# Kernel optimization log

Hardware: AMD Instinct MI355X
Metric: run time of the kernel (lower is better)

The kernel has to match this reference:

```python
import jax, jax.numpy as jnp
import numpy as np

HEAD_DIM = 256
ROTARY_DIM = 128  # max(2, int(0.5*256) rounded down to even)
HALF_ROT = ROTARY_DIM // 2   # 64
HALF_HEAD = HEAD_DIM // 2    # 128
WAVELENGTH = 10000.0
ROPE_SCALING = 1.0
SOFT_CAP = 50.0
EPS = 1e-6
NQ = 8
NKV = 4
GROUPS = NQ // NKV
NEG_INF = -1e9


def rms_norm(x, scale):
    # keras-hub Gemma RMSNorm: fp32 compute, out = x * rsqrt(mean(x^2)+eps) * (1+scale)
    x32 = x.astype(jnp.float32)
    var = jnp.mean(jnp.square(x32), axis=-1, keepdims=True)
    y = x32 * jax.lax.rsqrt(var + EPS)
    return (y * (1.0 + scale.astype(jnp.float32))).astype(x.dtype)


def l2_norm(x):
    # Gemma4VNorm: pure L2 normalization over head_dim, no learned scale
    x32 = x.astype(jnp.float32)
    ss = jnp.sum(jnp.square(x32), axis=-1, keepdims=True)
    return (x32 * jax.lax.rsqrt(ss + EPS)).astype(x.dtype)


def apply_partial_rope(x):
    # x: [B, S, N, HEAD_DIM]. Partial proportional rotation: only the first
    # HALF_ROT elements of each HALF_HEAD half get rotated. RoPE inverse freqs
    # use denominator_dim = HEAD_DIM (not rotary_dim).
    S = x.shape[1]
    inv_freq = 1.0 / (WAVELENGTH ** (jnp.arange(0, ROTARY_DIM, 2, dtype=jnp.float32) / HEAD_DIM))  # [HALF_ROT]
    pos = jnp.arange(S, dtype=jnp.float32) / ROPE_SCALING
    freq = pos[:, None] * inv_freq[None, :]             # [S, HALF_ROT]
    cos = jnp.cos(freq)[None, :, None, :].astype(x.dtype)
    sin = jnp.sin(freq)[None, :, None, :].astype(x.dtype)
    x1 = x[..., :HALF_HEAD]
    x2 = x[..., HALF_HEAD:]
    x1r, x1n = x1[..., :HALF_ROT], x1[..., HALF_ROT:]
    x2r, x2n = x2[..., :HALF_ROT], x2[..., HALF_ROT:]
    # rotate-half form: [x1r, x2r]*cos + [-x2r, x1r]*sin
    y1r = x1r * cos - x2r * sin
    y2r = x2r * cos + x1r * sin
    return jnp.concatenate([y1r, x1n, y2r, x2n], axis=-1)


def setup_inputs() -> dict:
    key = jax.random.key(0)
    ks = jax.random.split(key, 6)
    B, S, D = 2, 2048, 2048
    x = jax.random.normal(ks[0], (B, S, D), jnp.float32)
    # causal mask [B, S, S]
    attention_mask = jnp.broadcast_to(jnp.tril(jnp.ones((S, S), bool))[None], (B, S, S))
    w_scale = 0.02
    Wq = jax.random.normal(ks[1], (NQ, D, HEAD_DIM), jnp.float32) * w_scale
    Wk = jax.random.normal(ks[2], (NKV, D, HEAD_DIM), jnp.float32) * w_scale
    Wv = jax.random.normal(ks[3], (NKV, D, HEAD_DIM), jnp.float32) * w_scale
    Wo = jax.random.normal(ks[4], (NQ, HEAD_DIM, D), jnp.float32) * w_scale
    q_scale = jnp.zeros((HEAD_DIM,), jnp.float32)
    k_scale = jnp.zeros((HEAD_DIM,), jnp.float32)
    return {"x": x, "attention_mask": attention_mask, "Wq": Wq, "Wk": Wk,
            "Wv": Wv, "Wo": Wo, "q_scale": q_scale, "k_scale": k_scale}


def reference(x, attention_mask, Wq, Wk, Wv, Wo, q_scale, k_scale):
    B, S, D = x.shape
    q = jnp.einsum('btd,ndh->btnh', x, Wq)
    q = apply_partial_rope(rms_norm(q, q_scale))
    k = jnp.einsum('bsd,kdh->bskh', x, Wk)
    k = apply_partial_rope(rms_norm(k, k_scale))
    v = l2_norm(jnp.einsum('bsd,kdh->bskh', x, Wv))
    # grouped-query attention, scaling = 1.0 (Gemma4 relies on QK norm)
    qg = q.reshape(B, S, NKV, GROUPS, HEAD_DIM)
    logits = jnp.einsum('btkgh,bskh->bkgts', qg, k)
    # logit soft cap
    logits = jnp.tanh(logits / SOFT_CAP) * SOFT_CAP
    mask = attention_mask[:, None, None, :, :]
    logits = jnp.where(mask, logits, NEG_INF)
    probs = jax.nn.softmax(logits.astype(jnp.float32), axis=-1).astype(logits.dtype)
    out = jnp.einsum('bkgts,bskh->btkgh', probs, v).reshape(B, S, NQ, HEAD_DIM)
    return jnp.einsum('btnh,nhd->btd', out, Wo)
```

## Files before the change

kernel.cpp:

```cpp
#include <hip/hip_runtime.h>

#define AS1 __attribute__((address_space(1)))
#define AS3 __attribute__((address_space(3)))

typedef __attribute__((ext_vector_type(8))) _Float16 f16x8;
typedef __attribute__((ext_vector_type(4))) _Float16 f16x4;
typedef __attribute__((ext_vector_type(4))) float f32x4;

#define MFMA_K16(a, b, c) __builtin_amdgcn_mfma_f32_16x16x16f16(a, b, c, 0, 0, 0)

__device__ __forceinline__ unsigned short f2h(float f) {
    union { _Float16 h; unsigned short u; } v; v.h = (_Float16)f; return v.u;
}

__device__ __forceinline__ void gload16(const void* g, void* l) {
    __builtin_amdgcn_global_load_lds((const AS1 unsigned int*)g, (AS3 unsigned int*)l, 16, 0, 0);
}

#define GBAR() __builtin_amdgcn_s_barrier()
#define VM4()  asm volatile("s_waitcnt vmcnt(4)" ::: "memory")
#define VM0()  asm volatile("s_waitcnt vmcnt(0)" ::: "memory")

__global__ __launch_bounds__(256) void k_prep(const float* __restrict__ x,
                                              const float* __restrict__ Wq,
                                              const float* __restrict__ Wk,
                                              const float* __restrict__ Wv,
                                              const float* __restrict__ Wo,
                                              unsigned short* __restrict__ xh,
                                              unsigned short* __restrict__ WT,
                                              unsigned short* __restrict__ WoT) {
    int z = blockIdx.z;
    if (z == 24) {
        int blk = blockIdx.y * 8 + blockIdx.x;
        int t = threadIdx.y * 32 + threadIdx.x;
        const float4* s4 = (const float4*)x;
        ushort4* d4 = (ushort4*)xh;
        int base = blk * 4096 + t;
#pragma unroll
        for (int i = 0; i < 16; i++) {
            float4 v = s4[base + i * 256];
            ushort4 u;
            u.x = f2h(v.x); u.y = f2h(v.y); u.z = f2h(v.z); u.w = f2h(v.w);
            d4[base + i * 256] = u;
        }
        return;
    }
    const float* src; unsigned short* dst;
    int ld_src, c0, r0;
    if (z < 16) {
        if (z < 8)       { src = Wq + (size_t)z * 524288;        dst = WT + (size_t)z * 524288; }
        else if (z < 12) { src = Wk + (size_t)(z - 8) * 524288;  dst = WT + (size_t)2048 * 2048 + (size_t)(z - 8) * 524288; }
        else             { src = Wv + (size_t)(z - 12) * 524288; dst = WT + (size_t)3072 * 2048 + (size_t)(z - 12) * 524288; }
        ld_src = 256;
        c0 = blockIdx.x * 32; r0 = blockIdx.y * 32;
    } else {
        src = Wo; dst = WoT; ld_src = 2048;
        c0 = ((z - 16) * 8 + blockIdx.x) * 32; r0 = blockIdx.y * 32;
    }
    __shared__ float tile[32][33];
    int tx = threadIdx.x, ty = threadIdx.y;
#pragma unroll
    for (int i = 0; i < 4; i++)
        tile[ty + i * 8][tx] = src[(size_t)(r0 + ty + i * 8) * ld_src + c0 + tx];
    __syncthreads();
#pragma unroll
    for (int i = 0; i < 4; i++)
        dst[(size_t)(c0 + ty + i * 8) * 2048 + r0 + tx] = f2h(tile[tx][ty + i * 8]);
}

__global__ __launch_bounds__(256) void k_transpose_cvt(const float* __restrict__ src,
                                                       unsigned short* __restrict__ dst,
                                                       int ld_src, int ld_dst,
                                                       long zs_src, long zs_dst) {
    __shared__ float tile[32][33];
    long sb = (long)blockIdx.z * zs_src;
    long db = (long)blockIdx.z * zs_dst;
    int c0 = blockIdx.x * 32, r0 = blockIdx.y * 32;
    int tx = threadIdx.x, ty = threadIdx.y;
#pragma unroll
    for (int i = 0; i < 4; i++)
        tile[ty + i * 8][tx] = src[sb + (long)(r0 + ty + i * 8) * ld_src + c0 + tx];
    __syncthreads();
#pragma unroll
    for (int i = 0; i < 4; i++)
        dst[db + (long)(c0 + ty + i * 8) * ld_dst + r0 + tx] = f2h(tile[tx][ty + i * 8]);
}

template<int BUF, int MIH>
__device__ __forceinline__ void rdA(const unsigned short* SA, int wm, int fr, int g,
                                    f16x8 (&af)[4][2]) {
#pragma unroll
    for (int m = 0; m < 4; m++)
#pragma unroll
        for (int kk = 0; kk < 2; kk++) {
            int pos = wm * 64 + m * 16 + fr;
            af[m][kk] = *(const f16x8*)(SA + BUF * 16384 + MIH * 8192 + pos * 64 +
                                        (((kk * 4 + g) ^ (fr & 7)) << 3));
        }
}

template<int BUF, int NIH>
__device__ __forceinline__ void rdB(const unsigned short* SB, int wn, int fr, int g,
                                    f16x8 (&bf)[2][2]) {
#pragma unroll
    for (int ni2 = 0; ni2 < 2; ni2++)
#pragma unroll
        for (int kk = 0; kk < 2; kk++) {
            int pos = wn * 32 + ni2 * 16 + fr;
            bf[ni2][kk] = *(const f16x8*)(SB + BUF * 16384 + NIH * 8192 + pos * 64 +
                                          (((kk * 4 + g) ^ (fr & 7)) << 3));
        }
}

template<int MIH, int NIH>
__device__ __forceinline__ void mm16(f16x8 (&af)[4][2], f16x8 (&bf)[2][2], f32x4 (&acc)[8][4]) {
    __builtin_amdgcn_s_setprio(1);
#pragma unroll
    for (int m = 0; m < 4; m++)
#pragma unroll
        for (int ni2 = 0; ni2 < 2; ni2++)
#pragma unroll
            for (int kk = 0; kk < 2; kk++)
                acc[MIH * 4 + m][NIH * 2 + ni2] = __builtin_amdgcn_mfma_f32_16x16x32_f16(
                    af[m][kk], bf[ni2][kk], acc[MIH * 4 + m][NIH * 2 + ni2], 0, 0, 0);
    __builtin_amdgcn_s_setprio(0);
}

__global__ __launch_bounds__(512, 1) void k_gemm256(const unsigned short* __restrict__ A,
                                                    const unsigned short* __restrict__ Bt,
                                                    float* __restrict__ C,
                                                    int M, int N, int K, int nbx) {
    __shared__ __align__(16) unsigned short sm[65536];
    unsigned short* SA = sm;
    unsigned short* SB = sm + 32768;

    int tid = threadIdx.x, lane = tid & 63, wid = tid >> 6;
    int g = lane >> 4, fr = lane & 15;
    int wm = wid >> 2, wn = wid & 3;

    int bid = blockIdx.x;
    int sid = (bid & 7) * ((int)gridDim.x >> 3) + (bid >> 3);
    int by = sid / nbx, bx = sid % nbx;
    int rowA0 = by * 256, colB0 = bx * 256;

    f32x4 acc[8][4];
#pragma unroll
    for (int mi = 0; mi < 8; mi++)
#pragma unroll
        for (int ni = 0; ni < 4; ni++) acc[mi][ni] = (f32x4){0.f, 0.f, 0.f, 0.f};

    auto stA = [&](int buf, int h, int kt) {
#pragma unroll
        for (int t = 0; t < 2; t++) {
            int i = t * 512 + tid;
            int pos = i >> 3;
            int grow = rowA0 + ((pos >> 6) << 7) + h * 64 + (pos & 63);
            int cg = (i & 7) ^ (pos & 7);
            gload16(A + (size_t)grow * K + kt * 64 + cg * 8,
                    SA + buf * 16384 + h * 8192 + pos * 64 + (i & 7) * 8);
        }
    };
    auto stB = [&](int buf, int h, int kt) {
#pragma unroll
        for (int t = 0; t < 2; t++) {
            int i = t * 512 + tid;
            int pos = i >> 3;
            int gcol = colB0 + ((pos >> 5) << 6) + h * 32 + (pos & 31);
            int cg = (i & 7) ^ (pos & 7);
            gload16(Bt + (size_t)gcol * K + kt * 64 + cg * 8,
                    SB + buf * 16384 + h * 8192 + pos * 64 + (i & 7) * 8);
        }
    };

    int nT = K >> 6;
    stA(0, 0, 0); stB(0, 0, 0); stA(0, 1, 0); stB(0, 1, 0);
    stA(1, 0, 1); stB(1, 0, 1);
    VM4();
    GBAR();

    f16x8 af[4][2], bf[2][2];
    int nIt = nT >> 1;
    for (int it = 0; it < nIt; it++) {
        int T = it * 2;
        bool s36 = (T + 2 < nT), s78 = (T + 3 < nT);
        rdA<0, 0>(SA, wm, fr, g, af); rdB<0, 0>(SB, wn, fr, g, bf);
        stA(1, 1, T + 1);
        GBAR(); mm16<0, 0>(af, bf, acc); GBAR();
        rdB<0, 1>(SB, wn, fr, g, bf);
        stB(1, 1, T + 1);
        GBAR(); mm16<0, 1>(af, bf, acc); GBAR();
        rdA<0, 1>(SA, wm, fr, g, af); rdB<0, 0>(SB, wn, fr, g, bf);
        if (s36) stA(0, 0, T + 2);
        GBAR(); mm16<1, 0>(af, bf, acc); GBAR();
        rdB<0, 1>(SB, wn, fr, g, bf);
        if (s36) { stB(0, 0, T + 2); VM4(); } else { VM0(); }
        GBAR(); mm16<1, 1>(af, bf, acc); GBAR();
        rdA<1, 0>(SA, wm, fr, g, af); rdB<1, 0>(SB, wn, fr, g, bf);
        if (s36) stA(0, 1, T + 2);
        GBAR(); mm16<0, 0>(af, bf, acc); GBAR();
        rdB<1, 1>(SB, wn, fr, g, bf);
        if (s36) stB(0, 1, T + 2);
        GBAR(); mm16<0, 1>(af, bf, acc); GBAR();
        rdA<1, 1>(SA, wm, fr, g, af); rdB<1, 0>(SB, wn, fr, g, bf);
        if (s78) stA(1, 0, T + 3);
        GBAR(); mm16<1, 0>(af, bf, acc); GBAR();
        rdB<1, 1>(SB, wn, fr, g, bf);
        if (s78) { stB(1, 0, T + 3); VM4(); } else { VM0(); }
        GBAR(); mm16<1, 1>(af, bf, acc); GBAR();
    }

#pragma unroll
    for (int mi = 0; mi < 8; mi++) {
        int row = rowA0 + wm * 128 + mi * 16 + g * 4;
#pragma unroll
        for (int ni = 0; ni < 4; ni++) {
            int col = colB0 + wn * 64 + ni * 16 + fr;
#pragma unroll
            for (int r = 0; r < 4; r++)
                C[(size_t)(row + r) * N + col] = acc[mi][ni][r];
        }
    }
}

__global__ __launch_bounds__(256) void k_gemm_f16(const unsigned short* __restrict__ A,
                                                  const unsigned short* __restrict__ Bt,
                                                  float* __restrict__ C,
                                                  int M, int N, int K) {
    __shared__ unsigned short As[128 * 64];
    __shared__ unsigned short Bs[128 * 64];
    int tid = threadIdx.x;
    int lane = tid & 63, wid = tid >> 6;
    int g = lane >> 4, fr = lane & 15;
    int rowA0 = blockIdx.y * 128;
    int colB0 = blockIdx.x * 128;

    f32x4 zero = {0.f, 0.f, 0.f, 0.f};
    f32x4 acc[4][4];
#pragma unroll
    for (int mi = 0; mi < 4; mi++)
#pragma unroll
        for (int ni = 0; ni < 4; ni++) acc[mi][ni] = zero;

    const unsigned short* ag[4];
    const unsigned short* bg[4];
#pragma unroll
    for (int j = 0; j < 4; j++) {
        int id = j * 256 + tid;
        int r = id >> 3;
        int c = (id & 7) ^ (r & 7);
        ag[j] = A + (size_t)(rowA0 + r) * K + c * 8;
        bg[j] = Bt + (size_t)(colB0 + r) * K + c * 8;
    }

    int nK = K >> 6;
    for (int kt = 0; kt < nK; kt++) {
#pragma unroll
        for (int j = 0; j < 4; j++) {
            int id = j * 256 + tid;
            gload16(ag[j], As + id * 8);
            gload16(bg[j], Bs + id * 8);
            ag[j] += 64; bg[j] += 64;
        }
        __syncthreads();
#pragma unroll
        for (int kk = 0; kk < 2; kk++) {
            f16x8 af[4], bfr[4];
#pragma unroll
            for (int mi = 0; mi < 4; mi++) {
                int r = (wid >> 1) * 64 + mi * 16 + fr;
                af[mi] = *(const f16x8*)(As + r * 64 + ((((kk << 2) + g) ^ (r & 7)) << 3));
            }
#pragma unroll
            for (int ni = 0; ni < 4; ni++) {
                int r = (wid & 1) * 64 + ni * 16 + fr;
                bfr[ni] = *(const f16x8*)(Bs + r * 64 + ((((kk << 2) + g) ^ (r & 7)) << 3));
            }
#pragma unroll
            for (int mi = 0; mi < 4; mi++)
#pragma unroll
                for (int ni = 0; ni < 4; ni++)
                    acc[mi][ni] = __builtin_amdgcn_mfma_f32_16x16x32_f16(af[mi], bfr[ni], acc[mi][ni], 0, 0, 0);
        }
        __syncthreads();
    }

#pragma unroll
    for (int mi = 0; mi < 4; mi++) {
        int row = rowA0 + (wid >> 1) * 64 + mi * 16 + g * 4;
#pragma unroll
        for (int ni = 0; ni < 4; ni++) {
            int col = colB0 + (wid & 1) * 64 + ni * 16 + fr;
#pragma unroll
            for (int r = 0; r < 4; r++)
                C[(size_t)(row + r) * N + col] = acc[mi][ni][r];
        }
    }
}

__global__ __launch_bounds__(256) void k_norm_rope(float* __restrict__ qkv,
                                                   const float* __restrict__ q_scale,
                                                   const float* __restrict__ k_scale,
                                                   unsigned short* __restrict__ Qh,
                                                   unsigned short* __restrict__ Kh) {
    __shared__ float Y[256];
    __shared__ float red[4];
    int blk = blockIdx.x;
    int bt = blk >> 4, slot = blk & 15;
    int b = bt >> 11, t = bt & 2047;
    int h = threadIdx.x;
    int lane = h & 63, wid = h >> 6;

    float x = qkv[(size_t)bt * 4096 + slot * 256 + h];
    float v = x * x;
#pragma unroll
    for (int m = 1; m < 64; m <<= 1) v += __shfl_xor(v, m);
    if (lane == 0) red[wid] = v;
    __syncthreads();
    float ss = red[0] + red[1] + red[2] + red[3];

    float y;
    if (slot < 12) {
        float fac = rsqrtf(ss * (1.0f / 256.0f) + 1e-6f);
        const float* sc = (slot < 8) ? q_scale : k_scale;
        y = x * fac * (1.0f + sc[h]);
    } else {
        float fac = rsqrtf(ss + 1e-6f);
        y = x * fac;
    }
    Y[h] = y;
    __syncthreads();

    if (slot < 12) {
        float out;
        int hm = h & 127;
        if (hm < 64) {
            float inv = exp2f(-(float)hm * 0.10381025296522993f);
            float fr = (float)t * inv;
            float s = sinf(fr), c = cosf(fr);
            float y1 = Y[hm], y2 = Y[128 + hm];
            out = (h < 128) ? (y1 * c - y2 * s) : (y2 * c + y1 * s);
        } else {
            out = y;
        }
        unsigned short hv = f2h(out);
        if (slot < 8)
            Qh[((size_t)(b * 8 + slot) * 2048 + t) * 256 + h] = hv;
        else
            Kh[((size_t)(b * 4 + (slot - 8)) * 2048 + t) * 256 + h] = hv;
    } else {
        qkv[(size_t)bt * 4096 + slot * 256 + h] = y;
    }
}

__global__ __launch_bounds__(512, 2) void k_attn(const unsigned short* __restrict__ Qhg,
                                                 const unsigned short* __restrict__ Khg,
                                                 const unsigned short* __restrict__ Vtg,
                                                 unsigned short* __restrict__ attn) {
    __shared__ __align__(16) unsigned short KV[65536];
    unsigned short* Ks = KV;
    unsigned short* Vs = KV + 32768;

    int id = blockIdx.x;
    int bkv = id & 7;
    int npar = (id >> 3) & 1;
    int qt = id >> 4;
    int b = bkv >> 2, kv = bkv & 3;
    int n = kv * 2 + npar;
    int bn = b * 8 + n;
    int nkt = 2 * qt + 2;

    int tid = threadIdx.x, lane = tid & 63, wid = tid >> 6;
    int g = lane >> 4, fr = lane & 15;
    int g4 = g * 4, s7 = fr & 7;
    int q0 = qt * 128 + wid * 16;

    const unsigned short* Kh = Khg + (size_t)bkv * 2048 * 256;
    const unsigned short* Vh = Vtg + (size_t)bkv * 256 * 2048;
    const unsigned short* Qb = Qhg + (size_t)bn * 2048 * 256;

    const unsigned short* kb[4];
    const unsigned short* vb[4];
    int sd[4];
#pragma unroll
    for (int t2 = 0; t2 < 4; t2++) {
        int c_ = t2 * 512 + tid;
        int r = c_ >> 5, c = (c_ & 31) ^ (r & 7);
        kb[t2] = Kh + (size_t)r * 256 + c * 8;
        int d = c_ >> 3, cv = (c_ & 7) ^ (d & 7);
        vb[t2] = Vh + (size_t)d * 2048 + cv * 8;
        sd[t2] = c_ * 8;
    }

    int krb[4], vsl[4];
#pragma unroll
    for (int t16 = 0; t16 < 4; t16++) {
        krb[t16] = (t16 * 16 + fr) * 256;
        vsl[t16] = (((t16 * 2 + (g >> 1)) ^ s7) << 3) + (g & 1) * 4;
    }

    const unsigned short* qrow = Qb + (size_t)(q0 + fr) * 256;
    f16x8 aq[8];
#pragma unroll
    for (int kk = 0; kk < 8; kk++) aq[kk] = *(const f16x8*)(qrow + kk * 32 + g * 8);

    f32x4 zero4 = {0.f, 0.f, 0.f, 0.f};
    f32x4 o[16];
#pragma unroll
    for (int i2 = 0; i2 < 16; i2++) o[i2] = zero4;
    float m_run = -1e30f;
    float l_run = 0.f;

    auto STAGE = [&](int bufi, int kt2) {
#pragma unroll
        for (int t2 = 0; t2 < 4; t2++) {
            gload16(kb[t2] + (size_t)kt2 * 16384, Ks + bufi * 16384 + sd[t2]);
            gload16(vb[t2] + kt2 * 64, Vs + bufi * 16384 + sd[t2]);
        }
    };

    STAGE(0, 0);
    __syncthreads();

    for (int kt = 0; kt < nkt; kt++) {
        int cur = kt & 1;
        if (kt + 1 < nkt) STAGE(cur ^ 1, kt + 1);

        const unsigned short* KH = Ks + cur * 16384;
        const unsigned short* VC = Vs + cur * 16384;
        int k0 = kt * 64;

        f32x4 se[4] = {zero4, zero4, zero4, zero4};
        __builtin_amdgcn_s_setprio(1);
#pragma unroll
        for (int kk = 0; kk < 8; kk++) {
#pragma unroll
            for (int t16 = 0; t16 < 4; t16++) {
                f16x8 bk = *(const f16x8*)(KH + krb[t16] + ((((kk << 2) + g) ^ s7) << 3));
                se[t16] = __builtin_amdgcn_mfma_f32_16x16x32_f16(bk, aq[kk], se[t16], 0, 0, 0);
            }
        }
        __builtin_amdgcn_s_setprio(0);

        int qg = q0 + fr;
        float p4[4][4];
        float ml = -1e30f;
#pragma unroll
        for (int t16 = 0; t16 < 4; t16++)
#pragma unroll
            for (int r = 0; r < 4; r++) {
                float s = se[t16][r];
                float e = __expf(0.04f * s);
                s = 50.f - 100.f * __builtin_amdgcn_rcpf(1.f + e);
                int key = k0 + t16 * 16 + g4 + r;
                if (key > qg) s = -1e9f;
                p4[t16][r] = s;
                ml = fmaxf(ml, s);
            }
        ml = fmaxf(ml, __shfl_xor(ml, 16));
        ml = fmaxf(ml, __shfl_xor(ml, 32));

        if (__any(ml > m_run + 8.f)) {
            float mnew = fmaxf(m_run, ml);
            float swl = __expf(m_run - mnew);
            m_run = mnew;
            l_run *= swl;
            float swr[4];
#pragma unroll
            for (int r = 0; r < 4; r++) swr[r] = __shfl(swl, g4 + r);
#pragma unroll
            for (int nt = 0; nt < 16; nt++)
#pragma unroll
                for (int r = 0; r < 4; r++) o[nt][r] *= swr[r];
        }

        f16x4 pf[4];
#pragma unroll
        for (int t16 = 0; t16 < 4; t16++)
#pragma unroll
            for (int r = 0; r < 4; r++) {
                float p = __expf(p4[t16][r] - m_run);
                l_run += p;
                pf[t16][r] = (_Float16)p;
            }

        __builtin_amdgcn_s_setprio(1);
#pragma unroll
        for (int nt = 0; nt < 16; nt++) {
            int dbase = (nt * 16 + fr) * 64;
#pragma unroll
            for (int t16 = 0; t16 < 4; t16++) {
                f16x4 bv = *(const f16x4*)(VC + dbase + vsl[t16]);
                o[nt] = MFMA_K16(pf[t16], bv, o[nt]);
            }
        }
        __builtin_amdgcn_s_setprio(0);
        __syncthreads();
    }

    float l2 = l_run + __shfl_xor(l_run, 16);
    l2 += __shfl_xor(l2, 32);
    float li = __builtin_amdgcn_rcpf(fmaxf(l2, 1e-30f));
    float lrow[4];
#pragma unroll
    for (int r = 0; r < 4; r++) lrow[r] = __shfl(li, g4 + r);
#pragma unroll
    for (int nt = 0; nt < 16; nt++)
#pragma unroll
        for (int r = 0; r < 4; r++) {
            int qr = q0 + g4 + r;
            attn[(size_t)(b * 2048 + qr) * 2048 + n * 256 + nt * 16 + fr] = f2h(o[nt][r] * lrow[r]);
        }
}

extern "C" void kernel_launch(void* const* d_in, const int* in_sizes, int n_in,
                              void* d_out, int out_size, void* d_ws, size_t ws_size,
                              hipStream_t stream) {
    const float* x       = (const float*)d_in[0];
    const float* Wq      = (const float*)d_in[2];
    const float* Wk      = (const float*)d_in[3];
    const float* Wv      = (const float*)d_in[4];
    const float* Wo      = (const float*)d_in[5];
    const float* q_scale = (const float*)d_in[6];
    const float* k_scale = (const float*)d_in[7];
    float* out = (float*)d_out;
    char* ws = (char*)d_ws;

    const size_t MB = 1024 * 1024;
    unsigned short* xh    = (unsigned short*)ws;
    unsigned short* Qh    = (unsigned short*)ws;
    unsigned short* WT    = (unsigned short*)(ws + 16 * MB);
    unsigned short* Kh    = (unsigned short*)(ws + 16 * MB);
    unsigned short* Vt    = (unsigned short*)(ws + 24 * MB);
    unsigned short* WoT   = (unsigned short*)(ws + 32 * MB);
    float*          qkv   = (float*)(ws + 40 * MB);
    unsigned short* attnb = (unsigned short*)(ws + 40 * MB);

    dim3 tb(32, 8);
    k_prep<<<dim3(8, 64, 25), tb, 0, stream>>>(x, Wq, Wk, Wv, Wo, xh, WT, WoT);

    k_gemm256<<<dim3(256), dim3(512), 0, stream>>>(xh, WT, qkv, 4096, 4096, 2048, 16);
    k_norm_rope<<<dim3(65536), dim3(256), 0, stream>>>(qkv, q_scale, k_scale, Qh, Kh);
    for (int b = 0; b < 2; b++)
        k_transpose_cvt<<<dim3(8, 64, 4), tb, 0, stream>>>(qkv + (size_t)b * 2048 * 4096 + 3072,
                                                           Vt + (size_t)b * 4 * 256 * 2048,
                                                           4096, 2048, 256L, 524288L);
    k_attn<<<dim3(256), dim3(512), 0, stream>>>(Qh, Kh, Vt, attnb);

    k_gemm_f16<<<dim3(16, 32), dim3(256), 0, stream>>>(attnb, WoT, out, 4096, 2048, 2048);
}
```

Baseline: 309.4 us.

## Restructure attention into 64-row query tiles with split-key waves and merge

The attention kernel now runs 512 blocks of 256 threads, each covering a 64-row query tile. Tiles are paired as j and 31-j across the two launch halves to balance causal work. Each wave handles 32 query rows and one half of each 64-key tile, and the two key halves are merged at the end through shared memory using the stored max and sum. This adds partial-result storage and extra barriers. It also drops the double-buffered K/V prefetch in favour of a single buffer loaded synchronously each iteration, which exposes load latency. Each K/V fragment now feeds two query subtiles, raising register reuse.

```diff
diff --git a/kernel.cpp b/kernel.cpp
--- a/kernel.cpp
+++ b/kernel.cpp
@@ -8,6 +8,7 @@
 typedef __attribute__((ext_vector_type(4))) float f32x4;
 
 #define MFMA_K16(a, b, c) __builtin_amdgcn_mfma_f32_16x16x16f16(a, b, c, 0, 0, 0)
+#define MFMA_K32(a, b, c) __builtin_amdgcn_mfma_f32_16x16x32_f16(a, b, c, 0, 0, 0)
 
 __device__ __forceinline__ unsigned short f2h(float f) {
     union { _Float16 h; unsigned short u; } v; v.h = (_Float16)f; return v.u;
@@ -121,8 +122,8 @@
         for (int ni2 = 0; ni2 < 2; ni2++)
 #pragma unroll
             for (int kk = 0; kk < 2; kk++)
-                acc[MIH * 4 + m][NIH * 2 + ni2] = __builtin_amdgcn_mfma_f32_16x16x32_f16(
-                    af[m][kk], bf[ni2][kk], acc[MIH * 4 + m][NIH * 2 + ni2], 0, 0, 0);
+                acc[MIH * 4 + m][NIH * 2 + ni2] = MFMA_K32(af[m][kk], bf[ni2][kk],
+                                                           acc[MIH * 4 + m][NIH * 2 + ni2]);
     __builtin_amdgcn_s_setprio(0);
 }
 
@@ -279,7 +280,7 @@
             for (int mi = 0; mi < 4; mi++)
 #pragma unroll
                 for (int ni = 0; ni < 4; ni++)
-                    acc[mi][ni] = __builtin_amdgcn_mfma_f32_16x16x32_f16(af[mi], bfr[ni], acc[mi][ni], 0, 0, 0);
+                    acc[mi][ni] = MFMA_K32(af[mi], bfr[ni], acc[mi][ni]);
         }
         __syncthreads();
     }
@@ -352,164 +353,222 @@
     }
 }
 
-__global__ __launch_bounds__(512, 2) void k_attn(const unsigned short* __restrict__ Qhg,
+__global__ __launch_bounds__(256, 2) void k_attn(const unsigned short* __restrict__ Qhg,
                                                  const unsigned short* __restrict__ Khg,
                                                  const unsigned short* __restrict__ Vtg,
                                                  unsigned short* __restrict__ attn) {
-    __shared__ __align__(16) unsigned short KV[65536];
-    unsigned short* Ks = KV;
-    unsigned short* Vs = KV + 32768;
+    __shared__ __align__(16) char smem[66560];
+    unsigned short* Ks = (unsigned short*)smem;
+    unsigned short* Vs = (unsigned short*)(smem + 32768);
+    float* X  = (float*)smem;
+    float* ML = (float*)(smem + 65536);
 
     int id = blockIdx.x;
     int bkv = id & 7;
     int npar = (id >> 3) & 1;
-    int qt = id >> 4;
+    int pairidx = (id >> 4) & 15;
+    int half = id >> 8;
     int b = bkv >> 2, kv = bkv & 3;
     int n = kv * 2 + npar;
     int bn = b * 8 + n;
-    int nkt = 2 * qt + 2;
+    int j = half ? 31 - pairidx : pairidx;
+    int nkt = j + 1;
 
     int tid = threadIdx.x, lane = tid & 63, wid = tid >> 6;
+    int rg = wid >> 1, kh = wid & 1;
     int g = lane >> 4, fr = lane & 15;
     int g4 = g * 4, s7 = fr & 7;
-    int q0 = qt * 128 + wid * 16;
+    int q0 = j * 64 + rg * 32;
 
     const unsigned short* Kh = Khg + (size_t)bkv * 2048 * 256;
     const unsigned short* Vh = Vtg + (size_t)bkv * 256 * 2048;
     const unsigned short* Qb = Qhg + (size_t)bn * 2048 * 256;
 
-    const unsigned short* kb[4];
-    const unsigned short* vb[4];
-    int sd[4];
-#pragma unroll
-    for (int t2 = 0; t2 < 4; t2++) {
-        int c_ = t2 * 512 + tid;
-        int r = c_ >> 5, c = (c_ & 31) ^ (r & 7);
-        kb[t2] = Kh + (size_t)r * 256 + c * 8;
+    f16x8 bq[2][8];
+#pragma unroll
+    for (int qsub = 0; qsub < 2; qsub++) {
+        const unsigned short* qrow = Qb + (size_t)(q0 + qsub * 16 + fr) * 256;
+#pragma unroll
+        for (int kk = 0; kk < 8; kk++)
+            bq[qsub][kk] = *(const f16x8*)(qrow + kk * 32 + g * 8);
+    }
+
+    int koff[8], voff[8];
+#pragma unroll
+    for (int t2 = 0; t2 < 8; t2++) {
+        int c_ = t2 * 256 + tid;
+        int key = c_ >> 5, ck = (c_ & 31) ^ (key & 7);
+        koff[t2] = key * 256 + ck * 8;
         int d = c_ >> 3, cv = (c_ & 7) ^ (d & 7);
-        vb[t2] = Vh + (size_t)d * 2048 + cv * 8;
-        sd[t2] = c_ * 8;
-    }
-
-    int krb[4], vsl[4];
-#pragma unroll
-    for (int t16 = 0; t16 < 4; t16++) {
-        krb[t16] = (t16 * 16 + fr) * 256;
-        vsl[t16] = (((t16 * 2 + (g >> 1)) ^ s7) << 3) + (g & 1) * 4;
-    }
-
-    const unsigned short* qrow = Qb + (size_t)(q0 + fr) * 256;
-    f16x8 aq[8];
-#pragma unroll
-    for (int kk = 0; kk < 8; kk++) aq[kk] = *(const f16x8*)(qrow + kk * 32 + g * 8);
+        voff[t2] = d * 2048 + cv * 8;
+    }
+
+    int krb[2];
+#pragma unroll
+    for (int t16 = 0; t16 < 2; t16++) krb[t16] = (kh * 32 + t16 * 16 + fr) * 256;
+    int vsl[2];
+#pragma unroll
+    for (int t16 = 0; t16 < 2; t16++)
+        vsl[t16] = (((kh * 4 + t16 * 2 + (g >> 1)) ^ s7) << 3) + (g & 1) * 4;
 
     f32x4 zero4 = {0.f, 0.f, 0.f, 0.f};
-    f32x4 o[16];
-#pragma unroll
-    for (int i2 = 0; i2 < 16; i2++) o[i2] = zero4;
-    float m_run = -1e30f;
-    float l_run = 0.f;
-
-    auto STAGE = [&](int bufi, int kt2) {
-#pragma unroll
-        for (int t2 = 0; t2 < 4; t2++) {
-            gload16(kb[t2] + (size_t)kt2 * 16384, Ks + bufi * 16384 + sd[t2]);
-            gload16(vb[t2] + kt2 * 64, Vs + bufi * 16384 + sd[t2]);
-        }
-    };
-
-    STAGE(0, 0);
-    __syncthreads();
+    f32x4 o[2][16];
+#pragma unroll
+    for (int qsub = 0; qsub < 2; qsub++)
+#pragma unroll
+        for (int i2 = 0; i2 < 16; i2++) o[qsub][i2] = zero4;
+    float m_run[2] = {-1e30f, -1e30f};
+    float l_run[2] = {0.f, 0.f};
 
     for (int kt = 0; kt < nkt; kt++) {
-        int cur = kt & 1;
-        if (kt + 1 < nkt) STAGE(cur ^ 1, kt + 1);
-
-        const unsigned short* KH = Ks + cur * 16384;
-        const unsigned short* VC = Vs + cur * 16384;
         int k0 = kt * 64;
-
-        f32x4 se[4] = {zero4, zero4, zero4, zero4};
+#pragma unroll
+        for (int t2 = 0; t2 < 8; t2++) {
+            int c_ = t2 * 256 + tid;
+            gload16(Kh + (size_t)k0 * 256 + koff[t2], Ks + c_ * 8);
+            gload16(Vh + k0 + voff[t2], Vs + c_ * 8);
+        }
+        __syncthreads();
+
+        f32x4 se[2][2] = {{zero4, zero4}, {zero4, zero4}};
         __builtin_amdgcn_s_setprio(1);
 #pragma unroll
         for (int kk = 0; kk < 8; kk++) {
-#pragma unroll
-            for (int t16 = 0; t16 < 4; t16++) {
-                f16x8 bk = *(const f16x8*)(KH + krb[t16] + ((((kk << 2) + g) ^ s7) << 3));
-                se[t16] = __builtin_amdgcn_mfma_f32_16x16x32_f16(bk, aq[kk], se[t16], 0, 0, 0);
+            int co = ((((kk << 2) + g) ^ s7) << 3);
+            f16x8 bk0 = *(const f16x8*)(Ks + krb[0] + co);
+            f16x8 bk1 = *(const f16x8*)(Ks + krb[1] + co);
+            se[0][0] = MFMA_K32(bk0, bq[0][kk], se[0][0]);
+            se[1][0] = MFMA_K32(bk0, bq[1][kk], se[1][0]);
+            se[0][1] = MFMA_K32(bk1, bq[0][kk], se[0][1]);
+            se[1][1] = MFMA_K32(bk1, bq[1][kk], se[1][1]);
+        }
+        __builtin_amdgcn_s_setprio(0);
+
+        float p4[2][2][4];
+        float ml2[2] = {-1e30f, -1e30f};
+#pragma unroll
+        for (int qsub = 0; qsub < 2; qsub++) {
+            int qg = q0 + qsub * 16 + fr;
+#pragma unroll
+            for (int t16 = 0; t16 < 2; t16++)
+#pragma unroll
+                for (int r = 0; r < 4; r++) {
+                    float s = se[qsub][t16][r];
+                    float e = __expf(0.04f * s);
+                    s = 50.f - 100.f * __builtin_amdgcn_rcpf(1.f + e);
+                    int key = k0 + kh * 32 + t16 * 16 + g4 + r;
+                    if (key > qg) s = -1e9f;
+                    p4[qsub][t16][r] = s;
+                    ml2[qsub] = fmaxf(ml2[qsub], s);
+                }
+        }
+#pragma unroll
+        for (int qsub = 0; qsub < 2; qsub++) {
+            ml2[qsub] = fmaxf(ml2[qsub], __shfl_xor(ml2[qsub], 16));
+            ml2[qsub] = fmaxf(ml2[qsub], __shfl_xor(ml2[qsub], 32));
+        }
+
+        int needs = (ml2[0] > m_run[0] + 8.f) || (ml2[1] > m_run[1] + 8.f);
+        if (__any(needs)) {
+#pragma unroll
+            for (int qsub = 0; qsub < 2; qsub++) {
+                float mnew = fmaxf(m_run[qsub], ml2[qsub]);
+                float swl = __expf(m_run[qsub] - mnew);
+                m_run[qsub] = mnew;
+                l_run[qsub] *= swl;
+                float swr[4];
+#pragma unroll
+                for (int r = 0; r < 4; r++) swr[r] = __shfl(swl, g4 + r);
+#pragma unroll
+                for (int nt = 0; nt < 16; nt++)
+#pragma unroll
+                    for (int r = 0; r < 4; r++) o[qsub][nt][r] *= swr[r];
             }
         }
-        __builtin_amdgcn_s_setprio(0);
-
-        int qg = q0 + fr;
-        float p4[4][4];
-        float ml = -1e30f;
-#pragma unroll
-        for (int t16 = 0; t16 < 4; t16++)
-#pragma unroll
-            for (int r = 0; r < 4; r++) {
-                float s = se[t16][r];
-                float e = __expf(0.04f * s);
-                s = 50.f - 100.f * __builtin_amdgcn_rcpf(1.f + e);
-                int key = k0 + t16 * 16 + g4 + r;
-                if (key > qg) s = -1e9f;
-                p4[t16][r] = s;
-                ml = fmaxf(ml, s);
-            }
-        ml = fmaxf(ml, __shfl_xor(ml, 16));
-        ml = fmaxf(ml, __shfl_xor(ml, 32));
-
-        if (__any(ml > m_run + 8.f)) {
-            float mnew = fmaxf(m_run, ml);
-            float swl = __expf(m_run - mnew);
-            m_run = mnew;
-            l_run *= swl;
-            float swr[4];
-#pragma unroll
-            for (int r = 0; r < 4; r++) swr[r] = __shfl(swl, g4 + r);
-#pragma unroll
-            for (int nt = 0; nt < 16; nt++)
-#pragma unroll
-                for (int r = 0; r < 4; r++) o[nt][r] *= swr[r];
-        }
-
-        f16x4 pf[4];
-#pragma unroll
-        for (int t16 = 0; t16 < 4; t16++)
-#pragma unroll
-            for (int r = 0; r < 4; r++) {
-                float p = __expf(p4[t16][r] - m_run);
-                l_run += p;
-                pf[t16][r] = (_Float16)p;
-            }
+
+        f16x4 pf[2][2];
+#pragma unroll
+        for (int qsub = 0; qsub < 2; qsub++)
+#pragma unroll
+            for (int t16 = 0; t16 < 2; t16++)
+#pragma unroll
+                for (int r = 0; r < 4; r++) {
+                    float p = __expf(p4[qsub][t16][r] - m_run[qsub]);
+                    l_run[qsub] += p;
+                    pf[qsub][t16][r] = (_Float16)p;
+                }
 
         __builtin_amdgcn_s_setprio(1);
 #pragma unroll
         for (int nt = 0; nt < 16; nt++) {
             int dbase = (nt * 16 + fr) * 64;
-#pragma unroll
-            for (int t16 = 0; t16 < 4; t16++) {
-                f16x4 bv = *(const f16x4*)(VC + dbase + vsl[t16]);
-                o[nt] = MFMA_K16(pf[t16], bv, o[nt]);
-            }
+            f16x4 bv0 = *(const f16x4*)(Vs + dbase + vsl[0]);
+            f16x4 bv1 = *(const f16x4*)(Vs + dbase + vsl[1]);
+            o[0][nt] = MFMA_K16(pf[0][0], bv0, o[0][nt]);
+            o[1][nt] = MFMA_K16(pf[1][0], bv0, o[1][nt]);
+            o[0][nt] = MFMA_K16(pf[0][1], bv1, o[0][nt]);
+            o[1][nt] = MFMA_K16(pf[1][1], bv1, o[1][nt]);
         }
         __builtin_amdgcn_s_setprio(0);
         __syncthreads();
     }
 
-    float l2 = l_run + __shfl_xor(l_run, 16);
-    l2 += __shfl_xor(l2, 32);
-    float li = __builtin_amdgcn_rcpf(fmaxf(l2, 1e-30f));
-    float lrow[4];
-#pragma unroll
-    for (int r = 0; r < 4; r++) lrow[r] = __shfl(li, g4 + r);
-#pragma unroll
-    for (int nt = 0; nt < 16; nt++)
+    float l2[2];
+#pragma unroll
+    for (int qsub = 0; qsub < 2; qsub++) {
+        float l = l_run[qsub];
+        l += __shfl_xor(l, 16);
+        l += __shfl_xor(l, 32);
+        l2[qsub] = l;
+    }
+    if (lane < 16) {
+#pragma unroll
+        for (int qsub = 0; qsub < 2; qsub++) {
+            float* mp = ML + (((rg * 2 + kh) * 2 + qsub) * 16 + lane) * 2;
+            mp[0] = m_run[qsub]; mp[1] = l2[qsub];
+        }
+    }
+    __syncthreads();
+    float wr[2][4], lir[2][4];
+#pragma unroll
+    for (int qsub = 0; qsub < 2; qsub++) {
+        const float* mp = ML + (((rg * 2 + (kh ^ 1)) * 2 + qsub) * 16 + fr) * 2;
+        float mpv = mp[0], lpv = mp[1];
+        float ms = fmaxf(m_run[qsub], mpv);
+        float w = __expf(m_run[qsub] - ms);
+        float wp = __expf(mpv - ms);
+        float li = __builtin_amdgcn_rcpf(fmaxf(l2[qsub] * w + lpv * wp, 1e-30f));
 #pragma unroll
         for (int r = 0; r < 4; r++) {
-            int qr = q0 + g4 + r;
-            attn[(size_t)(b * 2048 + qr) * 2048 + n * 256 + nt * 16 + fr] = f2h(o[nt][r] * lrow[r]);
-        }
+            wr[qsub][r] = __shfl(w, g4 + r);
+            lir[qsub][r] = __shfl(li, g4 + r);
+        }
+    }
+    if (kh == 1) {
+#pragma unroll
+        for (int qsub = 0; qsub < 2; qsub++)
+#pragma unroll
+            for (int nt = 0; nt < 16; nt++)
+#pragma unroll
+                for (int r = 0; r < 4; r++)
+                    X[rg * 8192 + (qsub * 16 + g4 + r) * 256 + nt * 16 + fr] =
+                        o[qsub][nt][r] * wr[qsub][r];
+    }
+    __syncthreads();
+    if (kh == 0) {
+#pragma unroll
+        for (int qsub = 0; qsub < 2; qsub++)
+#pragma unroll
+            for (int nt = 0; nt < 16; nt++)
+#pragma unroll
+                for (int r = 0; r < 4; r++) {
+                    float val = (o[qsub][nt][r] * wr[qsub][r] +
+                                 X[rg * 8192 + (qsub * 16 + g4 + r) * 256 + nt * 16 + fr]) *
+                                lir[qsub][r];
+                    int qr = q0 + qsub * 16 + g4 + r;
+                    attn[(size_t)(b * 2048 + qr) * 2048 + n * 256 + nt * 16 + fr] = f2h(val);
+                }
+    }
 }
 
 extern "C" void kernel_launch(void* const* d_in, const int* in_sizes, int n_in,
@@ -544,7 +603,7 @@
         k_transpose_cvt<<<dim3(8, 64, 4), tb, 0, stream>>>(qkv + (size_t)b * 2048 * 4096 + 3072,
                                                            Vt + (size_t)b * 4 * 256 * 2048,
                                                            4096, 2048, 256L, 524288L);
-    k_attn<<<dim3(256), dim3(512), 0, stream>>>(Qh, Kh, Vt, attnb);
+    k_attn<<<dim3(512), dim3(256), 0, stream>>>(Qh, Kh, Vt, attnb);
 
     k_gemm_f16<<<dim3(16, 32), dim3(256), 0, stream>>>(attnb, WoT, out, 4096, 2048, 2048);
 }
```

Measured after the change: 297.5 us. 1.04x faster.
